# Performance work log

Hardware: AMD Instinct MI355X
Metric: run time of the kernel (lower is better)

The kernel has to match this reference:

```python
import jax, jax.numpy as jnp
import numpy as np

E = 1024      # embed_dim
H = 16        # num_heads
HD = E // H   # head_dim = 64
M = 64        # num_landmarks


def setup_inputs() -> dict:
    key = jax.random.key(0)
    ks = jax.random.split(key, 9)
    B, Lq, Lk = 2, 2048, 2048
    inv = 1.0 / np.sqrt(E)
    return {
        "query": jax.random.normal(ks[0], (B, Lq, E), dtype=jnp.float32),
        "key":   jax.random.normal(ks[1], (B, Lk, E), dtype=jnp.float32),
        "value": jax.random.normal(ks[2], (B, Lk, E), dtype=jnp.float32),
        # learned params (xavier-ish scale)
        "Wv": jax.random.normal(ks[3], (E, E), dtype=jnp.float32) * inv,
        "bv": jnp.zeros((E,), dtype=jnp.float32),
        "Wl": jax.random.normal(ks[4], (M, E), dtype=jnp.float32) * inv,
        "bl": jnp.zeros((M,), dtype=jnp.float32),
        "Wo": jax.random.normal(ks[5], (E, E), dtype=jnp.float32) * inv,
        "bo": jnp.zeros((E,), dtype=jnp.float32),
    }


def reference(query, key, value, Wv, bv, Wl, bl, Wo, bo):
    B, Lq, _ = query.shape
    Lk = key.shape[1]
    # value projection -> [B, H, Lk, HD]
    v = (value @ Wv.T + bv).reshape(B, Lk, H, HD).transpose(0, 2, 1, 3)
    # landmark projections + softmax over landmark dim
    ql = jax.nn.softmax((query @ Wl.T + bl) / np.sqrt(M), axis=-1)  # [B, Lq, M]
    kl = jax.nn.softmax((key @ Wl.T + bl) / np.sqrt(M), axis=-1)    # [B, Lk, M]
    # landmark attention: [B, Lq, Lk], scaled by sqrt(head_dim), softmax over keys
    attn = jax.nn.softmax(
        jnp.einsum("bqm,bkm->bqk", ql, kl) / np.sqrt(HD), axis=-1)
    # apply shared attention across heads: [B, H, Lq, HD]
    out_h = jnp.einsum("bqk,bhkd->bhqd", attn, v)
    out = out_h.transpose(0, 2, 1, 3).reshape(B, Lq, E)
    return out @ Wo.T + bo
```

## Files before the change

### kernel.cpp

```cpp
#include <hip/hip_runtime.h>
#include <hip/hip_bf16.h>
#include <cstdint>

typedef unsigned short u16;
typedef __attribute__((ext_vector_type(8))) short short8;
typedef __attribute__((ext_vector_type(4))) float f32x4;
typedef __attribute__((ext_vector_type(4))) unsigned short us4;

__device__ __forceinline__ u16 f2bf(float f) {
    union { float f; unsigned int i; } v; v.f = f;
    unsigned int x = v.i;
    unsigned int r = x + 0x7fffu + ((x >> 16) & 1u);
    return (u16)(r >> 16);
}

enum { EPI_F32 = 0, EPI_BF16 = 1, EPI_EXP_RS = 3, EPI_F32_DIV_CB = 4, EPI_LMSM = 5 };

template <int BM, int BN, int EPI, bool AF32, bool BF32>
__device__ __forceinline__ void gemm_body(
    char* __restrict__ smem,
    const void* __restrict__ Ax, const void* __restrict__ A2x,
    const void* __restrict__ Bx, void* __restrict__ Cv,
    int M, int N, int K, long sA, long sB, long sC,
    const float* __restrict__ biasCol, float* __restrict__ rowScale, float expScale,
    int m0, int n0, int z)
{
    constexpr int BK = 64;
    constexpr int MFRAG = (BM + 31) / 32;
    constexpr int NFRAG = BN / 32;
    constexpr int AG = (BM + 31) / 32;
    constexpr int BG = BN / 32;
    constexpr int TBUF = (BM + BN) * BK;

    const int tid = threadIdx.x;
    const int lane = tid & 63;
    const int quad = lane >> 4;
    const int l15 = lane & 15;
    const int w = tid >> 6;
    const int wm = w >> 1, wn = w & 1;

    const int r8 = tid >> 3;
    const int cl = tid & 7;
    const int cg = ((cl ^ (r8 & 7)) * 8);

    const u16* ap[AG];
    const float* apf[AG];
    if constexpr (AF32) {
        const float* base = (const float*)Ax;
        long mr = m0;
        if (A2x != nullptr && m0 >= (M >> 1)) { base = (const float*)A2x; mr = m0 - (M >> 1); }
        const float* Afb = base + (long)z * sA + (long)mr * K;
#pragma unroll
        for (int j = 0; j < AG; ++j) apf[j] = Afb + (long)(j * 32 + r8) * K + cg;
    } else {
        const u16* Ab = (const u16*)Ax + (long)z * sA + (long)m0 * K;
#pragma unroll
        for (int j = 0; j < AG; ++j) ap[j] = Ab + (long)(j * 32 + r8) * K + cg;
    }
    const u16* bp[BG];
    const float* bpf[BG];
    if constexpr (BF32) {
        const float* Bfb = (const float*)Bx + (long)z * sB + (long)n0 * K;
#pragma unroll
        for (int j = 0; j < BG; ++j) bpf[j] = Bfb + (long)(j * 32 + r8) * K + cg;
    } else {
        const u16* Bb = (const u16*)Bx + (long)z * sB + (long)n0 * K;
#pragma unroll
        for (int j = 0; j < BG; ++j) bp[j] = Bb + (long)(j * 32 + r8) * K + cg;
    }

    f32x4 acc[MFRAG][NFRAG] = {};
    const int sw = l15 & 7;
    u16* const base16 = (u16*)smem;
    const int NT = K / BK;

    {
        u16* As = base16;
        u16* Bs = base16 + BM * BK;
        if constexpr (!AF32) {
#pragma unroll
            for (int j = 0; j < AG; ++j) {
                __builtin_amdgcn_global_load_lds(
                    (const __attribute__((address_space(1))) void*)(ap[j]),
                    (__attribute__((address_space(3))) void*)(&As[(j * 32 + r8) * BK + cl * 8]),
                    16, 0, 0);
                ap[j] += BK;
            }
        } else {
#pragma unroll
            for (int j = 0; j < AG; ++j) {
                const float4 u0 = *(const float4*)(apf[j]);
                const float4 u1 = *(const float4*)(apf[j] + 4);
                short8 o;
                o[0] = (short)f2bf(u0.x); o[1] = (short)f2bf(u0.y);
                o[2] = (short)f2bf(u0.z); o[3] = (short)f2bf(u0.w);
                o[4] = (short)f2bf(u1.x); o[5] = (short)f2bf(u1.y);
                o[6] = (short)f2bf(u1.z); o[7] = (short)f2bf(u1.w);
                *(short8*)&As[(j * 32 + r8) * BK + cl * 8] = o;
                apf[j] += BK;
            }
        }
        if constexpr (!BF32) {
#pragma unroll
            for (int j = 0; j < BG; ++j) {
                __builtin_amdgcn_global_load_lds(
                    (const __attribute__((address_space(1))) void*)(bp[j]),
                    (__attribute__((address_space(3))) void*)(&Bs[(j * 32 + r8) * BK + cl * 8]),
                    16, 0, 0);
                bp[j] += BK;
            }
        } else {
#pragma unroll
            for (int j = 0; j < BG; ++j) {
                const float4 u0 = *(const float4*)(bpf[j]);
                const float4 u1 = *(const float4*)(bpf[j] + 4);
                short8 o;
                o[0] = (short)f2bf(u0.x); o[1] = (short)f2bf(u0.y);
                o[2] = (short)f2bf(u0.z); o[3] = (short)f2bf(u0.w);
                o[4] = (short)f2bf(u1.x); o[5] = (short)f2bf(u1.y);
                o[6] = (short)f2bf(u1.z); o[7] = (short)f2bf(u1.w);
                *(short8*)&Bs[(j * 32 + r8) * BK + cl * 8] = o;
                bpf[j] += BK;
            }
        }
    }
    __syncthreads();

    for (int t = 0; t < NT; ++t) {
        u16* Asc = base16 + (t & 1) * TBUF;
        u16* Bsc = Asc + BM * BK;
        u16* Asn = base16 + ((t + 1) & 1) * TBUF;
        u16* Bsn = Asn + BM * BK;
        const bool pf = (t + 1 < NT);

        float4 ra[AG][2];
        float4 rb[BG][2];
        if (pf) {
            if constexpr (!AF32) {
#pragma unroll
                for (int j = 0; j < AG; ++j) {
                    __builtin_amdgcn_global_load_lds(
                        (const __attribute__((address_space(1))) void*)(ap[j]),
                        (__attribute__((address_space(3))) void*)(&Asn[(j * 32 + r8) * BK + cl * 8]),
                        16, 0, 0);
                    ap[j] += BK;
                }
            } else {
#pragma unroll
                for (int j = 0; j < AG; ++j) {
                    ra[j][0] = *(const float4*)(apf[j]);
                    ra[j][1] = *(const float4*)(apf[j] + 4);
                    apf[j] += BK;
                }
            }
            if constexpr (!BF32) {
#pragma unroll
                for (int j = 0; j < BG; ++j) {
                    __builtin_amdgcn_global_load_lds(
                        (const __attribute__((address_space(1))) void*)(bp[j]),
                        (__attribute__((address_space(3))) void*)(&Bsn[(j * 32 + r8) * BK + cl * 8]),
                        16, 0, 0);
                    bp[j] += BK;
                }
            } else {
#pragma unroll
                for (int j = 0; j < BG; ++j) {
                    rb[j][0] = *(const float4*)(bpf[j]);
                    rb[j][1] = *(const float4*)(bpf[j] + 4);
                    bpf[j] += BK;
                }
            }
        }

#pragma unroll
        for (int ks = 0; ks < 2; ++ks) {
            short8 af[MFRAG], bfr[NFRAG];
#pragma unroll
            for (int i = 0; i < MFRAG; ++i)
                af[i] = *(const short8*)&Asc[(wm * (BM / 2) + i * 16 + l15) * BK +
                                             (((ks * 4 + quad) ^ sw) * 8)];
#pragma unroll
            for (int i = 0; i < NFRAG; ++i)
                bfr[i] = *(const short8*)&Bsc[(wn * (BN / 2) + i * 16 + l15) * BK +
                                              (((ks * 4 + quad) ^ sw) * 8)];
#pragma unroll
            for (int i = 0; i < MFRAG; ++i)
#pragma unroll
                for (int jn = 0; jn < NFRAG; ++jn)
                    acc[i][jn] = __builtin_amdgcn_mfma_f32_16x16x32_bf16(af[i], bfr[jn], acc[i][jn], 0, 0, 0);
        }

        if (pf) {
            if constexpr (AF32) {
#pragma unroll
                for (int j = 0; j < AG; ++j) {
                    short8 o;
                    o[0] = (short)f2bf(ra[j][0].x); o[1] = (short)f2bf(ra[j][0].y);
                    o[2] = (short)f2bf(ra[j][0].z); o[3] = (short)f2bf(ra[j][0].w);
                    o[4] = (short)f2bf(ra[j][1].x); o[5] = (short)f2bf(ra[j][1].y);
                    o[6] = (short)f2bf(ra[j][1].z); o[7] = (short)f2bf(ra[j][1].w);
                    *(short8*)&Asn[(j * 32 + r8) * BK + cl * 8] = o;
                }
            }
            if constexpr (BF32) {
#pragma unroll
                for (int j = 0; j < BG; ++j) {
                    short8 o;
                    o[0] = (short)f2bf(rb[j][0].x); o[1] = (short)f2bf(rb[j][0].y);
                    o[2] = (short)f2bf(rb[j][0].z); o[3] = (short)f2bf(rb[j][0].w);
                    o[4] = (short)f2bf(rb[j][1].x); o[5] = (short)f2bf(rb[j][1].y);
                    o[6] = (short)f2bf(rb[j][1].z); o[7] = (short)f2bf(rb[j][1].w);
                    *(short8*)&Bsn[(j * 32 + r8) * BK + cl * 8] = o;
                }
            }
        }
        __syncthreads();
    }

    if constexpr (EPI == EPI_LMSM) {
        float* red = (float*)(base16 + 2 * TBUF);
        float ev[4][NFRAG];
#pragma unroll
        for (int r = 0; r < 4; ++r) {
            float s = 0.f;
#pragma unroll
            for (int jn = 0; jn < NFRAG; ++jn) {
                const int col = wn * (BN / 2) + jn * 16 + l15;
                float v = exp2f((acc[0][jn][r] + biasCol[col]) * expScale);
                ev[r][jn] = v; s += v;
            }
            s += __shfl_xor(s, 1); s += __shfl_xor(s, 2);
            s += __shfl_xor(s, 4); s += __shfl_xor(s, 8);
            if (l15 == 0) red[wn * BM + wm * 16 + quad * 4 + r] = s;
        }
        __syncthreads();
#pragma unroll
        for (int r = 0; r < 4; ++r) {
            const int mrow = wm * 16 + quad * 4 + r;
            const float inv = 1.0f / (red[mrow] + red[BM + mrow]);
            const long m = m0 + mrow;
#pragma unroll
            for (int jn = 0; jn < NFRAG; ++jn) {
                const int col = wn * (BN / 2) + jn * 16 + l15;
                ((u16*)Cv)[m * N + col] = f2bf(ev[r][jn] * inv);
            }
        }
        return;
    } else {
#pragma unroll
        for (int i = 0; i < MFRAG; ++i) {
            const int mb = m0 + wm * (BM / 2) + i * 16 + quad * 4;
#pragma unroll
            for (int r = 0; r < 4; ++r) {
                const int m = mb + r;
                float rin = 0.f;
                if constexpr (EPI == EPI_F32_DIV_CB) rin = 1.0f / rowScale[(long)z * M + m];
                float rowsum = 0.f;
#pragma unroll
                for (int jn = 0; jn < NFRAG; ++jn) {
                    const int col = n0 + wn * (BN / 2) + jn * 16 + l15;
                    float v = acc[i][jn][r];
                    if constexpr (EPI == EPI_EXP_RS) { v = exp2f(v * expScale); rowsum += v; }
                    if constexpr (EPI == EPI_F32_DIV_CB) v = v * rin + biasCol[col];
                    if constexpr (EPI == EPI_F32 || EPI == EPI_F32_DIV_CB)
                        ((float*)Cv)[(long)z * sC + (long)m * N + col] = v;
                    else
                        ((u16*)Cv)[(long)z * sC + (long)m * N + col] = f2bf(v);
                }
                if constexpr (EPI == EPI_EXP_RS) {
                    rowsum += __shfl_xor(rowsum, 1);
                    rowsum += __shfl_xor(rowsum, 2);
                    rowsum += __shfl_xor(rowsum, 4);
                    rowsum += __shfl_xor(rowsum, 8);
                    if (l15 == 0) atomicAdd(&rowScale[(long)z * M + m], rowsum);
                }
            }
        }
    }
}

template <int BM, int BN, int EPI, bool AF32, bool BF32>
__global__ void __launch_bounds__(256)
gemm_bt(const void* __restrict__ Ax, const void* __restrict__ A2x,
        const void* __restrict__ Bx, void* __restrict__ Cv,
        int M, int N, int K, long sA, long sB, long sC,
        const float* __restrict__ biasCol, float* __restrict__ rowScale, float expScale)
{
    extern __shared__ char smem[];
    gemm_body<BM, BN, EPI, AF32, BF32>(smem, Ax, A2x, Bx, Cv, M, N, K, sA, sB, sC,
                                       biasCol, rowScale, expScale,
                                       blockIdx.y * BM, blockIdx.x * BN, blockIdx.z);
}

__global__ void __launch_bounds__(256)
fused23(const float* __restrict__ query, const float* __restrict__ key,
        const u16* __restrict__ Wlb, u16* __restrict__ qlkl,
        const float* __restrict__ bl,
        const float* __restrict__ Wo, const u16* __restrict__ WvT, u16* __restrict__ Wov)
{
    extern __shared__ char smem[];
    const int b = blockIdx.x;
    if (b < 256) {
        gemm_body<32, 64, EPI_LMSM, true, false>(smem, query, key, Wlb, qlkl,
            8192, 64, 1024, 0, 0, 0, bl, nullptr, 0.18033688011112042f,
            b * 32, 0, 0);
    } else {
        const int t = b - 256;
        gemm_body<64, 64, EPI_BF16, true, false>(smem, Wo, nullptr, WvT, Wov,
            1024, 1024, 1024, 0, 0, 0, nullptr, nullptr, 0.f,
            (t >> 4) * 64, (t & 15) * 64, 0);
    }
}

__global__ void __launch_bounds__(256)
fused45(const u16* __restrict__ Wov, const float* __restrict__ value, u16* __restrict__ Ut,
        const u16* __restrict__ qlkl, u16* __restrict__ Pm, float* __restrict__ rsc)
{
    extern __shared__ char smem[];
    const int b = blockIdx.x;
    if (b < 512) {
        const int x = b & 31, y = (b >> 5) & 7, z = b >> 8;
        gemm_body<128, 64, EPI_BF16, false, true>(smem, Wov, nullptr, value, Ut,
            1024, 2048, 1024, 0, 2097152, 2097152, nullptr, nullptr, 0.f,
            y * 128, x * 64, z);
    } else {
        const int t = b - 512;
        const int x = t & 15, y = (t >> 4) & 15, z = t >> 8;
        gemm_body<128, 128, EPI_EXP_RS, false, false>(smem, qlkl, nullptr, qlkl + 262144, Pm,
            2048, 2048, 64, 131072, 131072, 4194304, nullptr, rsc, 0.18033688011112042f,
            y * 128, x * 128, z);
    }
}

__global__ void __launch_bounds__(256)
prep_all(const float* __restrict__ Wl, const float* __restrict__ Wv,
         const float* __restrict__ Wo, const float* __restrict__ bv,
         const float* __restrict__ bo,
         u16* __restrict__ Wlb, u16* __restrict__ WvT,
         float* __restrict__ rsc, float* __restrict__ bocomb)
{
    __shared__ float t[64][65];
    const int b = blockIdx.x;
    const int tid = threadIdx.x;
    if (b < 64) {
        long i = ((long)b * 256 + tid) * 4;
        const float4 v = *(const float4*)(Wl + i);
        us4 o;
        o.x = f2bf(v.x); o.y = f2bf(v.y); o.z = f2bf(v.z); o.w = f2bf(v.w);
        *(us4*)(Wlb + i) = o;
    } else if (b < 320) {
        const int bidx = b - 64;
        const int bx = bidx & 15, by = bidx >> 4;
#pragma unroll
        for (int p = 0; p < 16; ++p) {
            int idx = p * 256 + tid;
            int r = idx >> 6, c = idx & 63;
            t[r][c] = Wv[(long)(by * 64 + r) * 1024 + bx * 64 + c];
        }
        __syncthreads();
#pragma unroll
        for (int p = 0; p < 16; ++p) {
            int idx = p * 256 + tid;
            int c = idx >> 6, r = idx & 63;
            WvT[(long)(bx * 64 + c) * 1024 + by * 64 + r] = f2bf(t[r][c]);
        }
        if (bx == 0) rsc[by * 256 + tid] = 0.f;
    } else {
        const int row = (b - 320) * 4 + (tid >> 6);
        const int lane = tid & 63;
        float s = 0.f;
#pragma unroll
        for (int i = 0; i < 16; ++i) s += Wo[(long)row * 1024 + i * 64 + lane] * bv[i * 64 + lane];
        for (int o = 32; o; o >>= 1) s += __shfl_xor(s, o, 64);
        if (lane == 0) bocomb[row] = bo[row] + s;
    }
}

extern "C" void kernel_launch(void* const* d_in, const int* in_sizes, int n_in,
                              void* d_out, int out_size, void* d_ws, size_t ws_size,
                              hipStream_t stream)
{
    const float* query = (const float*)d_in[0];
    const float* key   = (const float*)d_in[1];
    const float* value = (const float*)d_in[2];
    const float* Wv    = (const float*)d_in[3];
    const float* bv    = (const float*)d_in[4];
    const float* Wl    = (const float*)d_in[5];
    const float* bl    = (const float*)d_in[6];
    const float* Wo    = (const float*)d_in[7];
    const float* bo    = (const float*)d_in[8];
    float* out = (float*)d_out;

    char* ws = (char*)d_ws;
    u16*   Wlb    = (u16*)  (ws + 25165824);
    u16*   WvT    = (u16*)  (ws + 27394048);
    u16*   Wov    = (u16*)  (ws + 29491200);
    u16*   qlkl   = (u16*)  (ws + 31588352);
    u16*   Ut     = (u16*)  (ws + 32636928);
    u16*   Pm     = (u16*)  (ws + 41025536);
    float* rsc    = (float*)(ws + 57802752);
    float* bocomb = (float*)(ws + 57819136);

    prep_all<<<dim3(576), 256, 0, stream>>>(Wl, Wv, Wo, bv, bo,
                                            Wlb, WvT, rsc, bocomb);

    fused23<<<dim3(512), 256, 32768, stream>>>(query, key, Wlb, qlkl, bl,
                                               Wo, WvT, Wov);

    fused45<<<dim3(1024), 256, 49152, stream>>>(Wov, value, Ut, qlkl, Pm, rsc);

    gemm_bt<64, 128, EPI_F32_DIV_CB, false, false>
        <<<dim3(8, 32, 2), 256, 49152, stream>>>(
        Pm, nullptr, Ut, out, 2048, 1024, 2048,
        4194304, 2097152, 2097152, bocomb, rsc, 0.f);
}
```

Baseline: 165.8 us.

## Pipeline final GEMM with async LDS loads and redistribute prep work

Replaces the generic final Pm×Ut GEMM with a dedicated kernel that uses global_load_lds direct-to-LDS loads, a three-buffer ring with XOR swizzling, and vmcnt-based waits. This lets global loads overlap MFMA work. The prep kernel is also slimmed: Wl is read as fp32 directly inside the landmark GEMM, and the bias folding plus rsc zeroing move into extra blocks of fused23. The new kernel needs 72KB of dynamic shared memory, which may reduce occupancy, and it depends on the fixed shapes.

Result: no change. 166.2 us (+0.2%).

```diff
diff --git a/kernel.cpp b/kernel.cpp
--- a/kernel.cpp
+++ b/kernel.cpp
@@ -279,36 +279,150 @@
     }
 }
 
-template <int BM, int BN, int EPI, bool AF32, bool BF32>
 __global__ void __launch_bounds__(256)
-gemm_bt(const void* __restrict__ Ax, const void* __restrict__ A2x,
-        const void* __restrict__ Bx, void* __restrict__ Cv,
-        int M, int N, int K, long sA, long sB, long sC,
-        const float* __restrict__ biasCol, float* __restrict__ rowScale, float expScale)
+gemm6_pipe(const u16* __restrict__ Pm, const u16* __restrict__ Ut, float* __restrict__ out,
+           const float* __restrict__ bocomb, const float* __restrict__ rsc)
 {
     extern __shared__ char smem[];
-    gemm_body<BM, BN, EPI, AF32, BF32>(smem, Ax, A2x, Bx, Cv, M, N, K, sA, sB, sC,
-                                       biasCol, rowScale, expScale,
-                                       blockIdx.y * BM, blockIdx.x * BN, blockIdx.z);
+    constexpr int BK = 64, NT = 32;
+    constexpr int TB = (64 + 128) * BK;
+    const int tid = threadIdx.x;
+    const int lane = tid & 63;
+    const int quad = lane >> 4;
+    const int l15 = lane & 15;
+    const int w = tid >> 6;
+    const int wm = w >> 1, wn = w & 1;
+    const int z = blockIdx.z;
+    const int m0 = blockIdx.y * 64;
+    const int n0 = blockIdx.x * 128;
+
+    const int r8 = tid >> 3;
+    const int cl = tid & 7;
+    const int cg = ((cl ^ (r8 & 7)) * 8);
+
+    const u16* ap[2];
+    const u16* bp[4];
+    const u16* Ab = Pm + (long)z * 4194304 + (long)m0 * 2048;
+    const u16* Bb = Ut + (long)z * 2097152 + (long)n0 * 2048;
+#pragma unroll
+    for (int j = 0; j < 2; ++j) ap[j] = Ab + (long)(j * 32 + r8) * 2048 + cg;
+#pragma unroll
+    for (int j = 0; j < 4; ++j) bp[j] = Bb + (long)(j * 32 + r8) * 2048 + cg;
+
+    u16* const base16 = (u16*)smem;
+    auto stage = [&](int bi) {
+        u16* As = base16 + bi * TB;
+        u16* Bs = As + 64 * BK;
+#pragma unroll
+        for (int j = 0; j < 2; ++j) {
+            __builtin_amdgcn_global_load_lds(
+                (const __attribute__((address_space(1))) void*)(ap[j]),
+                (__attribute__((address_space(3))) void*)(&As[(j * 32 + r8) * BK + cl * 8]),
+                16, 0, 0);
+            ap[j] += BK;
+        }
+#pragma unroll
+        for (int j = 0; j < 4; ++j) {
+            __builtin_amdgcn_global_load_lds(
+                (const __attribute__((address_space(1))) void*)(bp[j]),
+                (__attribute__((address_space(3))) void*)(&Bs[(j * 32 + r8) * BK + cl * 8]),
+                16, 0, 0);
+            bp[j] += BK;
+        }
+    };
+
+    f32x4 acc[2][4] = {};
+    const int sw = l15 & 7;
+
+    stage(0);
+    stage(1);
+    asm volatile("s_waitcnt vmcnt(6)" ::: "memory");
+    __builtin_amdgcn_s_barrier();
+    __builtin_amdgcn_sched_barrier(0);
+
+    int cur = 0;
+    for (int t = 0; t < NT; ++t) {
+        int pre = cur + 2; if (pre >= 3) pre -= 3;
+        if (t + 2 < NT) stage(pre);
+
+        u16* Asc = base16 + cur * TB;
+        u16* Bsc = Asc + 64 * BK;
+#pragma unroll
+        for (int ks = 0; ks < 2; ++ks) {
+            short8 af[2], bfr[4];
+#pragma unroll
+            for (int i = 0; i < 2; ++i)
+                af[i] = *(const short8*)&Asc[(wm * 32 + i * 16 + l15) * BK +
+                                             (((ks * 4 + quad) ^ sw) * 8)];
+#pragma unroll
+            for (int i = 0; i < 4; ++i)
+                bfr[i] = *(const short8*)&Bsc[(wn * 64 + i * 16 + l15) * BK +
+                                              (((ks * 4 + quad) ^ sw) * 8)];
+#pragma unroll
+            for (int i = 0; i < 2; ++i)
+#pragma unroll
+                for (int jn = 0; jn < 4; ++jn)
+                    acc[i][jn] = __builtin_amdgcn_mfma_f32_16x16x32_bf16(af[i], bfr[jn], acc[i][jn], 0, 0, 0);
+        }
+
+        if (t + 2 < NT) {
+            asm volatile("s_waitcnt vmcnt(6)" ::: "memory");
+            __builtin_amdgcn_s_barrier();
+            __builtin_amdgcn_sched_barrier(0);
+        } else if (t + 1 < NT) {
+            asm volatile("s_waitcnt vmcnt(0)" ::: "memory");
+            __builtin_amdgcn_s_barrier();
+            __builtin_amdgcn_sched_barrier(0);
+        }
+        cur += 1; if (cur == 3) cur = 0;
+    }
+
+#pragma unroll
+    for (int i = 0; i < 2; ++i) {
+        const int mb = m0 + wm * 32 + i * 16 + quad * 4;
+#pragma unroll
+        for (int r = 0; r < 4; ++r) {
+            const int m = mb + r;
+            const float rin = 1.0f / rsc[z * 2048 + m];
+#pragma unroll
+            for (int jn = 0; jn < 4; ++jn) {
+                const int col = n0 + wn * 64 + jn * 16 + l15;
+                out[(long)z * 2097152 + (long)m * 1024 + col] =
+                    acc[i][jn][r] * rin + bocomb[col];
+            }
+        }
+    }
 }
 
 __global__ void __launch_bounds__(256)
 fused23(const float* __restrict__ query, const float* __restrict__ key,
-        const u16* __restrict__ Wlb, u16* __restrict__ qlkl,
+        const float* __restrict__ Wl, u16* __restrict__ qlkl,
         const float* __restrict__ bl,
-        const float* __restrict__ Wo, const u16* __restrict__ WvT, u16* __restrict__ Wov)
+        const float* __restrict__ Wo, const u16* __restrict__ WvT, u16* __restrict__ Wov,
+        const float* __restrict__ bv, const float* __restrict__ bo,
+        float* __restrict__ rsc, float* __restrict__ bocomb)
 {
     extern __shared__ char smem[];
     const int b = blockIdx.x;
     if (b < 256) {
-        gemm_body<32, 64, EPI_LMSM, true, false>(smem, query, key, Wlb, qlkl,
+        gemm_body<32, 64, EPI_LMSM, true, true>(smem, query, key, Wl, qlkl,
             8192, 64, 1024, 0, 0, 0, bl, nullptr, 0.18033688011112042f,
             b * 32, 0, 0);
-    } else {
+    } else if (b < 512) {
         const int t = b - 256;
         gemm_body<64, 64, EPI_BF16, true, false>(smem, Wo, nullptr, WvT, Wov,
             1024, 1024, 1024, 0, 0, 0, nullptr, nullptr, 0.f,
             (t >> 4) * 64, (t & 15) * 64, 0);
+    } else if (b < 768) {
+        const int row = (b - 512) * 4 + (threadIdx.x >> 6);
+        const int lane = threadIdx.x & 63;
+        float s = 0.f;
+#pragma unroll
+        for (int i = 0; i < 16; ++i) s += Wo[(long)row * 1024 + i * 64 + lane] * bv[i * 64 + lane];
+        for (int o = 32; o; o >>= 1) s += __shfl_xor(s, o, 64);
+        if (lane == 0) bocomb[row] = bo[row] + s;
+    } else {
+        rsc[(b - 768) * 256 + threadIdx.x] = 0.f;
     }
 }
 
@@ -333,46 +447,23 @@
 }
 
 __global__ void __launch_bounds__(256)
-prep_all(const float* __restrict__ Wl, const float* __restrict__ Wv,
-         const float* __restrict__ Wo, const float* __restrict__ bv,
-         const float* __restrict__ bo,
-         u16* __restrict__ Wlb, u16* __restrict__ WvT,
-         float* __restrict__ rsc, float* __restrict__ bocomb)
+prep_wvt(const float* __restrict__ Wv, u16* __restrict__ WvT)
 {
     __shared__ float t[64][65];
-    const int b = blockIdx.x;
+    const int bx = blockIdx.x & 15, by = blockIdx.x >> 4;
     const int tid = threadIdx.x;
-    if (b < 64) {
-        long i = ((long)b * 256 + tid) * 4;
-        const float4 v = *(const float4*)(Wl + i);
-        us4 o;
-        o.x = f2bf(v.x); o.y = f2bf(v.y); o.z = f2bf(v.z); o.w = f2bf(v.w);
-        *(us4*)(Wlb + i) = o;
-    } else if (b < 320) {
-        const int bidx = b - 64;
-        const int bx = bidx & 15, by = bidx >> 4;
-#pragma unroll
-        for (int p = 0; p < 16; ++p) {
-            int idx = p * 256 + tid;
-            int r = idx >> 6, c = idx & 63;
-            t[r][c] = Wv[(long)(by * 64 + r) * 1024 + bx * 64 + c];
-        }
-        __syncthreads();
-#pragma unroll
-        for (int p = 0; p < 16; ++p) {
-            int idx = p * 256 + tid;
-            int c = idx >> 6, r = idx & 63;
-            WvT[(long)(bx * 64 + c) * 1024 + by * 64 + r] = f2bf(t[r][c]);
-        }
-        if (bx == 0) rsc[by * 256 + tid] = 0.f;
-    } else {
-        const int row = (b - 320) * 4 + (tid >> 6);
-        const int lane = tid & 63;
-        float s = 0.f;
-#pragma unroll
-        for (int i = 0; i < 16; ++i) s += Wo[(long)row * 1024 + i * 64 + lane] * bv[i * 64 + lane];
-        for (int o = 32; o; o >>= 1) s += __shfl_xor(s, o, 64);
-        if (lane == 0) bocomb[row] = bo[row] + s;
+#pragma unroll
+    for (int p = 0; p < 16; ++p) {
+        int idx = p * 256 + tid;
+        int r = idx >> 6, c = idx & 63;
+        t[r][c] = Wv[(long)(by * 64 + r) * 1024 + bx * 64 + c];
+    }
+    __syncthreads();
+#pragma unroll
+    for (int p = 0; p < 16; ++p) {
+        int idx = p * 256 + tid;
+        int c = idx >> 6, r = idx & 63;
+        WvT[(long)(bx * 64 + c) * 1024 + by * 64 + r] = f2bf(t[r][c]);
     }
 }
 
@@ -392,7 +483,6 @@
     float* out = (float*)d_out;
 
     char* ws = (char*)d_ws;
-    u16*   Wlb    = (u16*)  (ws + 25165824);
     u16*   WvT    = (u16*)  (ws + 27394048);
     u16*   Wov    = (u16*)  (ws + 29491200);
     u16*   qlkl   = (u16*)  (ws + 31588352);
@@ -401,16 +491,19 @@
     float* rsc    = (float*)(ws + 57802752);
     float* bocomb = (float*)(ws + 57819136);
 
-    prep_all<<<dim3(576), 256, 0, stream>>>(Wl, Wv, Wo, bv, bo,
-                                            Wlb, WvT, rsc, bocomb);
-
-    fused23<<<dim3(512), 256, 32768, stream>>>(query, key, Wlb, qlkl, bl,
-                                               Wo, WvT, Wov);
+    static bool attr_done = false;
+    if (!attr_done) {
+        (void)hipFuncSetAttribute((const void*)gemm6_pipe,
+                                  hipFuncAttributeMaxDynamicSharedMemorySize, 73728);
+        attr_done = true;
+    }
+
+    prep_wvt<<<dim3(256), 256, 0, stream>>>(Wv, WvT);
+
+    fused23<<<dim3(784), 256, 32768, stream>>>(query, key, Wl, qlkl, bl,
+                                               Wo, WvT, Wov, bv, bo, rsc, bocomb);
 
     fused45<<<dim3(1024), 256, 49152, stream>>>(Wov, value, Ut, qlkl, Pm, rsc);
 
-    gemm_bt<64, 128, EPI_F32_DIV_CB, false, false>
-        <<<dim3(8, 32, 2), 256, 49152, stream>>>(
-        Pm, nullptr, Ut, out, 2048, 1024, 2048,
-        4194304, 2097152, 2097152, bocomb, rsc, 0.f);
-}
+    gemm6_pipe<<<dim3(8, 32, 2), 256, 73728, stream>>>(Pm, Ut, out, bocomb, rsc);
+}
```

## Project value directly instead of precomputing Wo·Wv, drop prep kernel

Applied to the files above, without the earlier changes.

The Wo·Wv weight-product precompute and the separate prep kernel (Wl bf16 cast, Wv transpose, bias fold, rsc zeroing) are removed. Instead the first fused kernel computes V2 = value·Wv^T straight from fp32 inputs, alongside the landmark projection, bias fold and rsc zeroing. The second kernel then multiplies Wo by V2 to form Ut. This cuts one launch and the prep traffic, but swaps a 1024^3 weight GEMM for a per-batch 2048x1024x1024 GEMM, and both now convert fp32 operands on load.

Result: slower. 201.2 us (+21.3%).

```diff
diff --git a/kernel.cpp b/kernel.cpp
--- a/kernel.cpp
+++ b/kernel.cpp
@@ -293,34 +293,48 @@
 }
 
 __global__ void __launch_bounds__(256)
-fused23(const float* __restrict__ query, const float* __restrict__ key,
-        const u16* __restrict__ Wlb, u16* __restrict__ qlkl,
-        const float* __restrict__ bl,
-        const float* __restrict__ Wo, const u16* __restrict__ WvT, u16* __restrict__ Wov)
+fusedA(const float* __restrict__ query, const float* __restrict__ key,
+       const float* __restrict__ Wl, u16* __restrict__ qlkl,
+       const float* __restrict__ bl,
+       const float* __restrict__ value, const float* __restrict__ Wv, u16* __restrict__ V2,
+       const float* __restrict__ Wo, const float* __restrict__ bv,
+       const float* __restrict__ bo,
+       float* __restrict__ rsc, float* __restrict__ bocomb)
 {
     extern __shared__ char smem[];
     const int b = blockIdx.x;
     if (b < 256) {
-        gemm_body<32, 64, EPI_LMSM, true, false>(smem, query, key, Wlb, qlkl,
+        gemm_body<32, 64, EPI_LMSM, true, true>(smem, query, key, Wl, qlkl,
             8192, 64, 1024, 0, 0, 0, bl, nullptr, 0.18033688011112042f,
             b * 32, 0, 0);
-    } else {
+    } else if (b < 768) {
         const int t = b - 256;
-        gemm_body<64, 64, EPI_BF16, true, false>(smem, Wo, nullptr, WvT, Wov,
-            1024, 1024, 1024, 0, 0, 0, nullptr, nullptr, 0.f,
-            (t >> 4) * 64, (t & 15) * 64, 0);
+        const int x = t & 15, y = (t >> 4) & 15, z = t >> 8;
+        gemm_body<128, 64, EPI_BF16, true, true>(smem, value, nullptr, Wv, V2,
+            2048, 1024, 1024, 2097152, 0, 2097152, nullptr, nullptr, 0.f,
+            y * 128, x * 64, z);
+    } else if (b < 1024) {
+        const int row = (b - 768) * 4 + (threadIdx.x >> 6);
+        const int lane = threadIdx.x & 63;
+        float s = 0.f;
+#pragma unroll
+        for (int i = 0; i < 16; ++i) s += Wo[(long)row * 1024 + i * 64 + lane] * bv[i * 64 + lane];
+        for (int o = 32; o; o >>= 1) s += __shfl_xor(s, o, 64);
+        if (lane == 0) bocomb[row] = bo[row] + s;
+    } else {
+        rsc[(b - 1024) * 256 + threadIdx.x] = 0.f;
     }
 }
 
 __global__ void __launch_bounds__(256)
-fused45(const u16* __restrict__ Wov, const float* __restrict__ value, u16* __restrict__ Ut,
-        const u16* __restrict__ qlkl, u16* __restrict__ Pm, float* __restrict__ rsc)
+fusedB(const float* __restrict__ Wo, const u16* __restrict__ V2, u16* __restrict__ Ut,
+       const u16* __restrict__ qlkl, u16* __restrict__ Pm, float* __restrict__ rsc)
 {
     extern __shared__ char smem[];
     const int b = blockIdx.x;
     if (b < 512) {
         const int x = b & 31, y = (b >> 5) & 7, z = b >> 8;
-        gemm_body<128, 64, EPI_BF16, false, true>(smem, Wov, nullptr, value, Ut,
+        gemm_body<128, 64, EPI_BF16, true, false>(smem, Wo, nullptr, V2, Ut,
             1024, 2048, 1024, 0, 2097152, 2097152, nullptr, nullptr, 0.f,
             y * 128, x * 64, z);
     } else {
@@ -329,50 +343,6 @@
         gemm_body<128, 128, EPI_EXP_RS, false, false>(smem, qlkl, nullptr, qlkl + 262144, Pm,
             2048, 2048, 64, 131072, 131072, 4194304, nullptr, rsc, 0.18033688011112042f,
             y * 128, x * 128, z);
-    }
-}
-
-__global__ void __launch_bounds__(256)
-prep_all(const float* __restrict__ Wl, const float* __restrict__ Wv,
-         const float* __restrict__ Wo, const float* __restrict__ bv,
-         const float* __restrict__ bo,
-         u16* __restrict__ Wlb, u16* __restrict__ WvT,
-         float* __restrict__ rsc, float* __restrict__ bocomb)
-{
-    __shared__ float t[64][65];
-    const int b = blockIdx.x;
-    const int tid = threadIdx.x;
-    if (b < 64) {
-        long i = ((long)b * 256 + tid) * 4;
-        const float4 v = *(const float4*)(Wl + i);
-        us4 o;
-        o.x = f2bf(v.x); o.y = f2bf(v.y); o.z = f2bf(v.z); o.w = f2bf(v.w);
-        *(us4*)(Wlb + i) = o;
-    } else if (b < 320) {
-        const int bidx = b - 64;
-        const int bx = bidx & 15, by = bidx >> 4;
-#pragma unroll
-        for (int p = 0; p < 16; ++p) {
-            int idx = p * 256 + tid;
-            int r = idx >> 6, c = idx & 63;
-            t[r][c] = Wv[(long)(by * 64 + r) * 1024 + bx * 64 + c];
-        }
-        __syncthreads();
-#pragma unroll
-        for (int p = 0; p < 16; ++p) {
-            int idx = p * 256 + tid;
-            int c = idx >> 6, r = idx & 63;
-            WvT[(long)(bx * 64 + c) * 1024 + by * 64 + r] = f2bf(t[r][c]);
-        }
-        if (bx == 0) rsc[by * 256 + tid] = 0.f;
-    } else {
-        const int row = (b - 320) * 4 + (tid >> 6);
-        const int lane = tid & 63;
-        float s = 0.f;
-#pragma unroll
-        for (int i = 0; i < 16; ++i) s += Wo[(long)row * 1024 + i * 64 + lane] * bv[i * 64 + lane];
-        for (int o = 32; o; o >>= 1) s += __shfl_xor(s, o, 64);
-        if (lane == 0) bocomb[row] = bo[row] + s;
     }
 }
 
@@ -392,22 +362,18 @@
     float* out = (float*)d_out;
 
     char* ws = (char*)d_ws;
-    u16*   Wlb    = (u16*)  (ws + 25165824);
-    u16*   WvT    = (u16*)  (ws + 27394048);
-    u16*   Wov    = (u16*)  (ws + 29491200);
+    u16*   V2     = (u16*)  (ws + 0);
     u16*   qlkl   = (u16*)  (ws + 31588352);
     u16*   Ut     = (u16*)  (ws + 32636928);
     u16*   Pm     = (u16*)  (ws + 41025536);
     float* rsc    = (float*)(ws + 57802752);
     float* bocomb = (float*)(ws + 57819136);
 
-    prep_all<<<dim3(576), 256, 0, stream>>>(Wl, Wv, Wo, bv, bo,
-                                            Wlb, WvT, rsc, bocomb);
-
-    fused23<<<dim3(512), 256, 32768, stream>>>(query, key, Wlb, qlkl, bl,
-                                               Wo, WvT, Wov);
-
-    fused45<<<dim3(1024), 256, 49152, stream>>>(Wov, value, Ut, qlkl, Pm, rsc);
+    fusedA<<<dim3(1040), 256, 49152, stream>>>(query, key, Wl, qlkl, bl,
+                                               value, Wv, V2, Wo, bv, bo,
+                                               rsc, bocomb);
+
+    fusedB<<<dim3(1024), 256, 49152, stream>>>(Wo, V2, Ut, qlkl, Pm, rsc);
 
     gemm_bt<64, 128, EPI_F32_DIV_CB, false, false>
         <<<dim3(8, 32, 2), 256, 49152, stream>>>(
```
